# Performance work log

Hardware: AMD Instinct MI355X
Metric: run time of the kernel (lower is better)

The kernel has to match this reference:

```python
import jax, jax.numpy as jnp
import numpy as np

B, T, F, H, P, HEADS = 1024, 128, 9, 256, 2048, 4
DH = H // HEADS

def _lstm_layer(x, Wih, Whh, bih, bhh):
    # x: [B,T,in]; gate order i,f,g,o (torch convention)
    xp = jnp.einsum('bti,gi->btg', x, Wih) + bih + bhh  # [B,T,4H]
    h0 = jnp.zeros((x.shape[0], Whh.shape[1]), x.dtype)
    def step(carry, xt):
        h, c = carry
        g = xt + h @ Whh.T
        i, f, gg, o = jnp.split(g, 4, axis=-1)
        c = jax.nn.sigmoid(f) * c + jax.nn.sigmoid(i) * jnp.tanh(gg)
        h = jax.nn.sigmoid(o) * jnp.tanh(c)
        return (h, c), h
    _, hs = jax.lax.scan(step, (h0, h0), jnp.swapaxes(xp, 0, 1))
    return jnp.swapaxes(hs, 0, 1)  # [B,T,H]

def _layernorm(x, g, b, eps=1e-5):
    mu = x.mean(-1, keepdims=True)
    var = ((x - mu) ** 2).mean(-1, keepdims=True)
    return (x - mu) * jax.lax.rsqrt(var + eps) * g + b

def setup_inputs():
    key = jax.random.key(0)
    ks = jax.random.split(key, 30)
    w = lambda k, s: jax.random.normal(k, s, jnp.float32) * 0.05
    return {
        'x': jax.random.normal(ks[0], (B, T, F), jnp.float32),
        'sku_indices': jnp.arange(B, dtype=jnp.int32),
        'adj': jax.random.uniform(ks[1], (P, P), jnp.float32),
        'vsn_emb_w': w(ks[2], (F, H)), 'vsn_emb_b': w(ks[3], (F, H)),
        'vsn_sel_w': w(ks[4], (F, F)), 'vsn_sel_b': w(ks[5], (F,)),
        'lstm_Wih0': w(ks[6], (4 * H, H)), 'lstm_Whh0': w(ks[7], (4 * H, H)),
        'lstm_bih0': w(ks[8], (4 * H,)), 'lstm_bhh0': w(ks[9], (4 * H,)),
        'lstm_Wih1': w(ks[10], (4 * H, H)), 'lstm_Whh1': w(ks[11], (4 * H, H)),
        'lstm_bih1': w(ks[12], (4 * H,)), 'lstm_bhh1': w(ks[13], (4 * H,)),
        'attn_in_w': w(ks[14], (3 * H, H)), 'attn_in_b': w(ks[15], (3 * H,)),
        'attn_out_w': w(ks[16], (H, H)), 'attn_out_b': w(ks[17], (H,)),
        'gnn_w': w(ks[18], (H, H)), 'gnn_b': w(ks[19], (H,)),
        'ln_g': jnp.ones((H,), jnp.float32), 'ln_b': jnp.zeros((H,), jnp.float32),
        'gate_w': w(ks[20], (H, 2 * H)), 'gate_b': w(ks[21], (H,)),
        'out_w': w(ks[22], (1, H)), 'out_b': w(ks[23], (1,)),
    }

def reference(x, sku_indices, adj, vsn_emb_w, vsn_emb_b, vsn_sel_w, vsn_sel_b,
              lstm_Wih0, lstm_Whh0, lstm_bih0, lstm_bhh0,
              lstm_Wih1, lstm_Whh1, lstm_bih1, lstm_bhh1,
              attn_in_w, attn_in_b, attn_out_w, attn_out_b,
              gnn_w, gnn_b, ln_g, ln_b, gate_w, gate_b, out_w, out_b):
    # --- TFT hidden: variable selection -> 2-layer LSTM -> MHA, take last step ---
    emb = x[..., None] * vsn_emb_w + vsn_emb_b           # [B,T,F,H]
    wts = jax.nn.softmax(x @ vsn_sel_w.T + vsn_sel_b, -1)  # [B,T,F]
    h = jnp.einsum('btf,btfh->bth', wts, emb)            # [B,T,H]
    h = _lstm_layer(h, lstm_Wih0, lstm_Whh0, lstm_bih0, lstm_bhh0)
    h = _lstm_layer(h, lstm_Wih1, lstm_Whh1, lstm_bih1, lstm_bhh1)
    qkv = h @ attn_in_w.T + attn_in_b                    # [B,T,3H]
    q, k, v = [a.reshape(B, T, HEADS, DH) for a in jnp.split(qkv, 3, axis=-1)]
    scores = jnp.einsum('bqhd,bkhd->bhqk', q, k) / np.sqrt(DH).astype(np.float32)
    attn = jax.nn.softmax(scores, -1)
    o = jnp.einsum('bhqk,bkhd->bqhd', attn, v).reshape(B, T, H)
    o = o @ attn_out_w.T + attn_out_b
    hidden = o[:, -1, :]                                  # [B,H]
    # --- GNN enrichment (all sku_indices valid here) ---
    product_embeds = jnp.zeros((P, H), hidden.dtype).at[sku_indices].set(hidden)
    degree = jnp.clip(adj.sum(1, keepdims=True), 1e-6)
    aggregated = (adj / degree) @ product_embeds          # [P,H]
    transformed = jax.nn.gelu(aggregated @ gnn_w.T + gnn_b, approximate=False)
    transformed = _layernorm(transformed, ln_g, ln_b)
    enriched = transformed[sku_indices]                   # [B,H]
    gate = jax.nn.sigmoid(jnp.concatenate([hidden, enriched], -1) @ gate_w.T + gate_b)
    combined = gate * enriched + (1.0 - gate) * hidden
    out = combined @ out_w.T + out_b                      # [B,1]
    return out.squeeze(-1)
```

## Files before the change

kernel.cpp:

```cpp
#include <hip/hip_runtime.h>
#include <hip/hip_fp16.h>

typedef _Float16 f16;
typedef _Float16 f16x8 __attribute__((ext_vector_type(8)));
typedef _Float16 f16x4 __attribute__((ext_vector_type(4)));
typedef float f32x4 __attribute__((ext_vector_type(4)));

#define B_ 1024
#define T_ 128
#define F_ 9
#define H_ 256
#define P_ 2048

typedef unsigned long long ull;
#define AL(p) __hip_atomic_load((p), __ATOMIC_RELAXED, __HIP_MEMORY_SCOPE_AGENT)
#define AS(p, v) __hip_atomic_store((p), (v), __ATOMIC_RELAXED, __HIP_MEMORY_SCOPE_AGENT)

__device__ __forceinline__ float sigf(float x) { return 1.f / (1.f + __expf(-x)); }
__device__ __forceinline__ float tanh_(float x) {
  float a = fminf(fabsf(x), 12.f);
  float e = __expf(2.f * a);
  float r = 1.f - 2.f / (e + 1.f);
  return copysignf(r, x);
}

__device__ __forceinline__ f16x8 aload16(const f16* p) {
  union { ull u[2]; f16x8 v; } r;
  r.u[0] = AL((const ull*)p);
  r.u[1] = AL((const ull*)p + 1);
  return r.v;
}

__device__ __forceinline__ float blk_sum(float v) {
  __shared__ float sh[8];
  int lane = threadIdx.x & 63, w = threadIdx.x >> 6;
  int nw = blockDim.x >> 6;
#pragma unroll
  for (int o = 32; o > 0; o >>= 1) v += __shfl_xor(v, o, 64);
  __syncthreads();
  if (lane == 0) sh[w] = v;
  __syncthreads();
  float t = 0.f;
  for (int i = 0; i < nw; i++) t += sh[i];
  return t;
}

__global__ __launch_bounds__(256) void gemm_f16(
    const f16* __restrict__ A, int lda,
    const f16* __restrict__ Bt, int ldb,
    const float* __restrict__ bias,
    f16* __restrict__ o16, int ldo16,
    float* __restrict__ o32, int ldo32,
    f16* __restrict__ o16t, int ldt,
    int M, int N, int K)
{
  __shared__ __align__(16) f16 As[128][40];
  __shared__ __align__(16) f16 Bs[128][40];
  const int tid = threadIdx.x;
  const int lane = tid & 63, wave = tid >> 6;
  const int wr = (wave >> 1) * 64, wc = (wave & 1) * 64;
  const int q = lane >> 4, l15 = lane & 15;
  const int bm = blockIdx.x * 128, bn = blockIdx.y * 128;

  f32x4 acc[4][4];
#pragma unroll
  for (int i = 0; i < 4; i++)
#pragma unroll
    for (int j = 0; j < 4; j++) acc[i][j] = (f32x4){0.f, 0.f, 0.f, 0.f};

  for (int k0 = 0; k0 < K; k0 += 32) {
#pragma unroll
    for (int c = 0; c < 2; ++c) {
      int ch = tid + c * 256;
      int row = ch >> 2, kh = (ch & 3) * 8;
      *(f16x8*)&As[row][kh] = *(const f16x8*)&A[(size_t)(bm + row) * lda + k0 + kh];
      *(f16x8*)&Bs[row][kh] = *(const f16x8*)&Bt[(size_t)(bn + row) * ldb + k0 + kh];
    }
    __syncthreads();
    f16x8 af[4], bf[4];
#pragma unroll
    for (int tm = 0; tm < 4; tm++) af[tm] = *(const f16x8*)&As[wr + tm * 16 + l15][q * 8];
#pragma unroll
    for (int tn = 0; tn < 4; tn++) bf[tn] = *(const f16x8*)&Bs[wc + tn * 16 + l15][q * 8];
#pragma unroll
    for (int tm = 0; tm < 4; tm++)
#pragma unroll
      for (int tn = 0; tn < 4; tn++)
        acc[tm][tn] = __builtin_amdgcn_mfma_f32_16x16x32_f16(af[tm], bf[tn], acc[tm][tn], 0, 0, 0);
    __syncthreads();
  }
#pragma unroll
  for (int tm = 0; tm < 4; tm++) {
#pragma unroll
    for (int tn = 0; tn < 4; tn++) {
      int colg = bn + wc + tn * 16 + l15;
      float bv = bias ? bias[colg] : 0.f;
#pragma unroll
      for (int r = 0; r < 4; r++) {
        int rowg = bm + wr + tm * 16 + q * 4 + r;
        float v = acc[tm][tn][r] + bv;
        if (o32) o32[(size_t)rowg * ldo32 + colg] = v;
        if (o16) o16[(size_t)rowg * ldo16 + colg] = (f16)v;
        if (o16t) o16t[(size_t)colg * ldt + rowg] = (f16)v;
      }
    }
  }
}

__global__ __launch_bounds__(256, 1) void lstm_pipe(
    f16* __restrict__ hio,
    const f16* __restrict__ wpk0, const f16* __restrict__ wpk1,
    const float* __restrict__ b0, const float* __restrict__ b1,
    int* __restrict__ cnt0, int* __restrict__ cnt1)
{
  __shared__ __align__(16) f16 apf[2][16][64][8];
  __shared__ __align__(16) f16 htile[32][64];
  const int tid = threadIdx.x;
  const int lane = tid & 63, w = tid >> 6;
  const int q = lane >> 4, l15 = lane & 15;
  const int layer = blockIdx.x >> 7;
  const int lbid = blockIdx.x & 127;
  const int grp = lbid & 31, s = lbid >> 5;
  const int m0 = grp * 32;
  const f16* wpk = layer ? wpk1 : wpk0;
  const float* bias = layer ? b1 : b0;
  int* myflags = (layer ? cnt1 : cnt0) + grp * 64;
  int* xflags  = cnt0 + grp * 64;

  const int own0 = ((w >> 1) == s);
  const int own1 = (((w + 4) >> 1) == s);
  const int offh = (w & 1) * 32;

  f16x8 bf[4][16];
  {
    const f16* wbase = wpk + (((size_t)(s * 4 + w) * 4) * 16) * 512 + lane * 8;
#pragma unroll
    for (int g = 0; g < 4; g++)
#pragma unroll
      for (int k = 0; k < 16; k++)
        bf[g][k] = *(const f16x8*)(wbase + (size_t)(g * 16 + k) * 512);
  }
  float bv[4];
#pragma unroll
  for (int g = 0; g < 4; g++) bv[g] = bias[g * 256 + s * 64 + w * 16 + l15];

  const int srow = lane & 15, scb = lane >> 4;
  size_t rb[2];
  rb[0] = ((size_t)(m0 + srow) * T_) * 256 + scb * 8;
  rb[1] = ((size_t)(m0 + 16 + srow) * T_) * 256 + scb * 8;

  const f16x8 zv = {(f16)0, (f16)0, (f16)0, (f16)0, (f16)0, (f16)0, (f16)0, (f16)0};

  if (layer) {
    if (tid == 0) {
      int it = 0;
      for (;;) {
        ull a = AL((ull*)xflags);
        ull b2 = AL((ull*)xflags + 1);
        if ((int)a >= 2 && (int)(a >> 32) >= 2 &&
            (int)b2 >= 2 && (int)(b2 >> 32) >= 2) break;
        __builtin_amdgcn_s_sleep(1);
        if (++it > (1 << 22)) break;
      }
    }
    __syncthreads();
  }
  f16x8 xr[2][2];
#pragma unroll
  for (int mt = 0; mt < 2; mt++) {
    if (layer) {
      xr[mt][0] = aload16(&hio[rb[mt] + (size_t)w * 32]);
      xr[mt][1] = aload16(&hio[rb[mt] + (size_t)(w + 4) * 32]);
    } else {
      xr[mt][0] = *(const f16x8*)&hio[rb[mt] + (size_t)w * 32];
      xr[mt][1] = *(const f16x8*)&hio[rb[mt] + (size_t)(w + 4) * 32];
    }
  }
  float cst[2][4] = {{0.f, 0.f, 0.f, 0.f}, {0.f, 0.f, 0.f, 0.f}};

  __syncthreads();
  if (tid == 0) AS(&myflags[s], 1);

  for (int t = 0; t < T_; ++t) {
    if (tid == 0) {
      const int needO = t + 1;
      int needX = 0;
      if (layer) { needX = t + 3; if (needX > T_ + 1) needX = T_ + 1; }
      int it = 0;
      for (;;) {
        ull a = AL((ull*)myflags);
        ull b2 = AL((ull*)myflags + 1);
        bool ok = (int)a >= needO && (int)(a >> 32) >= needO &&
                  (int)b2 >= needO && (int)(b2 >> 32) >= needO;
        if (ok && layer) {
          ull c = AL((ull*)xflags);
          ull d = AL((ull*)xflags + 1);
          ok = (int)c >= needX && (int)(c >> 32) >= needX &&
               (int)d >= needX && (int)(d >> 32) >= needX;
        }
        if (ok) break;
        __builtin_amdgcn_s_sleep(1);
        if (++it > (1 << 22)) break;
      }
    }
    __syncthreads();

#pragma unroll
    for (int mt = 0; mt < 2; mt++) {
      *(f16x8*)&apf[mt][w][lane][0]     = xr[mt][0];
      *(f16x8*)&apf[mt][w + 4][lane][0] = xr[mt][1];
      f16x8 h0 = zv, h1 = zv;
      if (t > 0) {
        if (own0) h0 = *(const f16x8*)&htile[mt * 16 + srow][offh + scb * 8];
        else      h0 = aload16(&hio[rb[mt] + (size_t)(t - 1) * 256 + (size_t)w * 32]);
        if (own1) h1 = *(const f16x8*)&htile[mt * 16 + srow][offh + scb * 8];
        else      h1 = aload16(&hio[rb[mt] + (size_t)(t - 1) * 256 + (size_t)(w + 4) * 32]);
      }
      *(f16x8*)&apf[mt][8 + w][lane][0]  = h0;
      *(f16x8*)&apf[mt][12 + w][lane][0] = h1;
    }
    __syncthreads();

    f32x4 acc[2][4];
#pragma unroll
    for (int mt = 0; mt < 2; mt++)
#pragma unroll
      for (int g = 0; g < 4; g++) acc[mt][g] = (f32x4){0.f, 0.f, 0.f, 0.f};
#pragma unroll
    for (int k = 0; k < 16; k++) {
      f16x8 a0 = *(const f16x8*)&apf[0][k][lane][0];
      f16x8 a1 = *(const f16x8*)&apf[1][k][lane][0];
#pragma unroll
      for (int g = 0; g < 4; g++) {
        acc[0][g] = __builtin_amdgcn_mfma_f32_16x16x32_f16(a0, bf[g][k], acc[0][g], 0, 0, 0);
        acc[1][g] = __builtin_amdgcn_mfma_f32_16x16x32_f16(a1, bf[g][k], acc[1][g], 0, 0, 0);
      }
    }
    if (t + 1 < T_) {
#pragma unroll
      for (int mt = 0; mt < 2; mt++) {
        if (layer) {
          xr[mt][0] = aload16(&hio[rb[mt] + (size_t)(t + 1) * 256 + (size_t)w * 32]);
          xr[mt][1] = aload16(&hio[rb[mt] + (size_t)(t + 1) * 256 + (size_t)(w + 4) * 32]);
        } else {
          xr[mt][0] = *(const f16x8*)&hio[rb[mt] + (size_t)(t + 1) * 256 + (size_t)w * 32];
          xr[mt][1] = *(const f16x8*)&hio[rb[mt] + (size_t)(t + 1) * 256 + (size_t)(w + 4) * 32];
        }
      }
    }
    f16 hn[2][4];
#pragma unroll
    for (int mt = 0; mt < 2; mt++)
#pragma unroll
      for (int r = 0; r < 4; r++) {
        float ip = acc[mt][0][r] + bv[0];
        float fp = acc[mt][1][r] + bv[1];
        float gp = acc[mt][2][r] + bv[2];
        float op = acc[mt][3][r] + bv[3];
        float cn = sigf(fp) * cst[mt][r] + sigf(ip) * tanh_(gp);
        cst[mt][r] = cn;
        hn[mt][r] = (f16)(sigf(op) * tanh_(cn));
      }
#pragma unroll
    for (int mt = 0; mt < 2; mt++)
#pragma unroll
      for (int r = 0; r < 4; r++)
        htile[mt * 16 + q * 4 + r][w * 16 + l15] = hn[mt][r];
    __syncthreads();
    {
      int row = tid >> 3, c8 = (tid & 7) * 8;
      union { ull u[2]; f16x8 v; } uh;
      uh.v = *(const f16x8*)&htile[row][c8];
      ull* dst =
          (ull*)&hio[((size_t)(m0 + row) * T_ + t) * 256 + s * 64 + c8];
      AS(dst, uh.u[0]);
      AS(dst + 1, uh.u[1]);
    }
    __syncthreads();
    if (tid == 0) AS(&myflags[s], t + 2);
  }
}

__global__ __launch_bounds__(256) void vsn_w_kernel(
    const float* __restrict__ x, const float* __restrict__ selw,
    const float* __restrict__ selb, float* __restrict__ wb)
{
  int pos = blockIdx.x * 256 + threadIdx.x;
  const float* xr = x + (size_t)pos * F_;
  float xv[F_];
#pragma unroll
  for (int f = 0; f < F_; f++) xv[f] = xr[f];
  float wv[F_]; float mx = -1e30f;
#pragma unroll
  for (int f = 0; f < F_; f++) {
    float s = selb[f];
#pragma unroll
    for (int f2 = 0; f2 < F_; f2++) s += xv[f2] * selw[f * F_ + f2];
    wv[f] = s; mx = fmaxf(mx, s);
  }
  float se = 0.f;
#pragma unroll
  for (int f = 0; f < F_; f++) { wv[f] = __expf(wv[f] - mx); se += wv[f]; }
  float inv = 1.f / se;
  float* o = wb + (size_t)pos * 18;
#pragma unroll
  for (int f = 0; f < F_; f++) {
    float wt = wv[f] * inv;
    o[f] = wt; o[9 + f] = wt * xv[f];
  }
}

__global__ __launch_bounds__(256) void vsn_h_kernel(
    const float* __restrict__ wb, const float* __restrict__ embw,
    const float* __restrict__ embb, f16* __restrict__ hout)
{
  int j = threadIdx.x;
  float ew[F_], eb[F_];
#pragma unroll
  for (int f = 0; f < F_; f++) { ew[f] = embw[f * H_ + j]; eb[f] = embb[f * H_ + j]; }
  for (int i = 0; i < 128; i++) {
    size_t pos = blockIdx.x + (size_t)i * 1024;
    const float* w = wb + pos * 18;
    float h = 0.f;
#pragma unroll
    for (int f = 0; f < F_; f++) h += w[9 + f] * ew[f] + w[f] * eb[f];
    hout[pos * H_ + j] = (f16)h;
  }
}

__global__ __launch_bounds__(256) void attn_fused_kernel(
    const f16* __restrict__ hseq, const float* __restrict__ qbuf,
    const float* __restrict__ attn_in_w, const float* __restrict__ attn_in_b,
    f16* __restrict__ aob)
{
  __shared__ __align__(16) f16 hs[T_][264];
  __shared__ float qs[256];
  __shared__ float qks[4][256];
  __shared__ float ps[4][T_];
  __shared__ float hb[4][256];
  int b = blockIdx.x, tid = threadIdx.x;
  for (int i = tid; i < T_ * 32; i += 256) {
    int row = i >> 5, cc = (i & 31) * 8;
    *(f16x8*)&hs[row][cc] = *(const f16x8*)&hseq[((size_t)b * T_ + row) * 256 + cc];
  }
  qs[tid] = qbuf[(size_t)b * 256 + tid];
  __syncthreads();
  {
    int j = tid;
#pragma unroll
    for (int h = 0; h < 4; h++) {
      float acc = 0.f;
      for (int d = 0; d < 64; d++)
        acc += qs[h * 64 + d] * attn_in_w[(size_t)(256 + h * 64 + d) * 256 + j];
      qks[h][j] = acc * 0.125f;
    }
  }
  __syncthreads();
  if (tid < T_) {
    float s[4] = {0.f, 0.f, 0.f, 0.f};
    for (int cc = 0; cc < 32; cc++) {
      f16x8 v = *(const f16x8*)&hs[tid][cc * 8];
#pragma unroll
      for (int h = 0; h < 4; h++) {
        float a = 0.f;
#pragma unroll
        for (int j = 0; j < 8; j++) a += qks[h][cc * 8 + j] * (float)v[j];
        s[h] += a;
      }
    }
#pragma unroll
    for (int h = 0; h < 4; h++) ps[h][tid] = s[h];
  }
  __syncthreads();
  {
    int w = tid >> 6, l = tid & 63;
    float a = ps[w][l], bb = ps[w][l + 64];
    float m = fmaxf(a, bb);
#pragma unroll
    for (int o = 32; o > 0; o >>= 1) m = fmaxf(m, __shfl_xor(m, o, 64));
    float e0 = __expf(a - m), e1 = __expf(bb - m);
    float se = e0 + e1;
#pragma unroll
    for (int o = 32; o > 0; o >>= 1) se += __shfl_xor(se, o, 64);
    float inv = 1.f / se;
    ps[w][l] = e0 * inv; ps[w][l + 64] = e1 * inv;
  }
  __syncthreads();
  {
    int j = tid;
    float acc[4] = {0.f, 0.f, 0.f, 0.f};
    for (int t = 0; t < T_; t++) {
      float hv = (float)hs[t][j];
#pragma unroll
      for (int h = 0; h < 4; h++) acc[h] += ps[h][t] * hv;
    }
#pragma unroll
    for (int h = 0; h < 4; h++) hb[h][j] = acc[h];
  }
  __syncthreads();
  {
    int d = tid, h = d >> 6;
    const float4* wr = (const float4*)(attn_in_w + (size_t)(512 + d) * 256);
    float acc = 0.f;
    for (int cc = 0; cc < 64; cc++) {
      float4 w4 = wr[cc];
      acc += w4.x * hb[h][cc * 4] + w4.y * hb[h][cc * 4 + 1]
           + w4.z * hb[h][cc * 4 + 2] + w4.w * hb[h][cc * 4 + 3];
    }
    aob[(size_t)b * 256 + d] = (f16)(acc + attn_in_b[512 + d]);
  }
}

__global__ __launch_bounds__(256) void deg_adjn_kernel(
    const float* __restrict__ adj, const int* __restrict__ sku,
    f16* __restrict__ adjn)
{
  int bp = blockIdx.x;
  int p = sku[bp];
  int tid = threadIdx.x;
  float s = 0.f;
  for (int j = tid; j < P_; j += 256) s += adj[(size_t)p * P_ + j];
  float tot = blk_sum(s);
  float inv = 1.f / fmaxf(tot, 1e-6f);
  for (int b = tid; b < B_; b += 256)
    adjn[(size_t)bp * B_ + b] = (f16)(adj[(size_t)p * P_ + sku[b]] * inv);
}

__global__ __launch_bounds__(256) void gelu_ln_kernel(
    const float* __restrict__ pre, const float* __restrict__ lg,
    const float* __restrict__ lb, float* __restrict__ enr,
    f16* __restrict__ hidcat)
{
  int row = blockIdx.x, j = threadIdx.x;
  float xv = pre[row * 256 + j];
  float ge = 0.5f * xv * (1.f + erff(xv * 0.70710678118654752f));
  float mu = blk_sum(ge) * (1.f / 256.f);
  float d = ge - mu;
  float var = blk_sum(d * d) * (1.f / 256.f);
  float y = d * rsqrtf(var + 1e-5f) * lg[j] + lb[j];
  enr[row * 256 + j] = y;
  hidcat[row * 512 + 256 + j] = (f16)y;
}

__global__ __launch_bounds__(256) void final_kernel(
    const float* __restrict__ gpre, const float* __restrict__ enr,
    const float* __restrict__ hid, const float* __restrict__ outw,
    const float* __restrict__ outb, float* __restrict__ out)
{
  int b = blockIdx.x, j = threadIdx.x;
  float gt = sigf(gpre[b * 256 + j]);
  float comb = gt * enr[b * 256 + j] + (1.f - gt) * hid[b * 256 + j];
  float v = comb * outw[j];
  float s = blk_sum(v);
  if (j == 0) out[b] = s + outb[0];
}

__global__ void prep_kernel(
    const float* Wih0, const float* Whh0, const float* Wih1, const float* Whh1,
    const float* bih0, const float* bhh0, const float* bih1, const float* bhh1,
    const float* attn_in_w, const float* attn_out_w, const float* gnn_w,
    const float* gate_w,
    f16* wpk0, f16* wpk1, f16* attninf, f16* attnoutf, f16* gnnwf, f16* gatewf,
    float* bias0, float* bias1, int* flagz)
{
  int idx = blockIdx.x * 256 + threadIdx.x;
  if (idx < 524288) {
    int j = idx & 7, lane = (idx >> 3) & 63, k = (idx >> 9) & 15;
    int g = (idx >> 13) & 3, w = (idx >> 15) & 3, s = (idx >> 17) & 3;
    int row = g * 256 + s * 64 + w * 16 + (lane & 15);
    int col = k * 32 + (lane >> 4) * 8 + j;
    float v0 = col < 256 ? Wih0[(size_t)row * 256 + col] : Whh0[(size_t)row * 256 + col - 256];
    float v1 = col < 256 ? Wih1[(size_t)row * 256 + col] : Whh1[(size_t)row * 256 + col - 256];
    wpk0[idx] = (f16)v0;
    wpk1[idx] = (f16)v1;
    return;
  }
  int i = idx - 524288;
  if (i < 65536) { attninf[i] = (f16)attn_in_w[i]; return; }
  i -= 65536;
  if (i < 65536) { attnoutf[i] = (f16)attn_out_w[i]; return; }
  i -= 65536;
  if (i < 65536) { gnnwf[i] = (f16)gnn_w[i]; return; }
  i -= 65536;
  if (i < 131072) { gatewf[i] = (f16)gate_w[i]; return; }
  i -= 131072;
  if (i < 1024) { bias0[i] = bih0[i] + bhh0[i]; return; }
  i -= 1024;
  if (i < 1024) { bias1[i] = bih1[i] + bhh1[i]; return; }
  i -= 1024;
  if (i < 4096) { flagz[i] = 0; return; }
}

extern "C" void kernel_launch(void* const* d_in, const int* in_sizes, int n_in,
                              void* d_out, int out_size, void* d_ws, size_t ws_size,
                              hipStream_t stream)
{
  const float* x         = (const float*)d_in[0];
  const int*   sku       = (const int*)  d_in[1];
  const float* adj       = (const float*)d_in[2];
  const float* vsn_emb_w = (const float*)d_in[3];
  const float* vsn_emb_b = (const float*)d_in[4];
  const float* vsn_sel_w = (const float*)d_in[5];
  const float* vsn_sel_b = (const float*)d_in[6];
  const float* Wih0 = (const float*)d_in[7];
  const float* Whh0 = (const float*)d_in[8];
  const float* bih0 = (const float*)d_in[9];
  const float* bhh0 = (const float*)d_in[10];
  const float* Wih1 = (const float*)d_in[11];
  const float* Whh1 = (const float*)d_in[12];
  const float* bih1 = (const float*)d_in[13];
  const float* bhh1 = (const float*)d_in[14];
  const float* attn_in_w  = (const float*)d_in[15];
  const float* attn_in_b  = (const float*)d_in[16];
  const float* attn_out_w = (const float*)d_in[17];
  const float* attn_out_b = (const float*)d_in[18];
  const float* gnn_w  = (const float*)d_in[19];
  const float* gnn_b  = (const float*)d_in[20];
  const float* ln_g   = (const float*)d_in[21];
  const float* ln_b   = (const float*)d_in[22];
  const float* gate_w = (const float*)d_in[23];
  const float* gate_b = (const float*)d_in[24];
  const float* out_w  = (const float*)d_in[25];
  const float* out_b  = (const float*)d_in[26];
  (void)in_sizes; (void)n_in; (void)out_size; (void)ws_size;

  char* wsb = (char*)d_ws;
  size_t off = 0;
  auto alloc = [&](size_t bytes) -> void* {
    void* p = wsb + off;
    off += (bytes + 255) & ~(size_t)255;
    return p;
  };
  f16* hA      = (f16*)alloc((size_t)B_ * T_ * H_ * 2);
  f16* wpk0    = (f16*)alloc((size_t)1024 * 512 * 2);
  f16* wpk1    = (f16*)alloc((size_t)1024 * 512 * 2);
  f16* attninf = (f16*)alloc((size_t)256 * 256 * 2);
  f16* attnoutf= (f16*)alloc((size_t)256 * 256 * 2);
  f16* gnnwf   = (f16*)alloc((size_t)256 * 256 * 2);
  f16* gatewf  = (f16*)alloc((size_t)256 * 512 * 2);
  float* bias0 = (float*)alloc(1024 * 4);
  float* bias1 = (float*)alloc(1024 * 4);
  int* cnt0    = (int*)alloc(32 * 64 * 4);
  int* cnt1    = (int*)alloc(32 * 64 * 4);
  size_t off_tail = off;
  float* qbuf  = (float*)alloc((size_t)B_ * 256 * 4);
  f16* aob     = (f16*)alloc((size_t)B_ * 256 * 2);
  float* hidden32 = (float*)alloc((size_t)B_ * 256 * 4);
  f16* hidcat  = (f16*)alloc((size_t)B_ * 512 * 2);
  f16* hT      = (f16*)alloc((size_t)256 * B_ * 2);
  f16* adjn    = (f16*)alloc((size_t)B_ * B_ * 2);
  f16* aggf    = (f16*)alloc((size_t)B_ * 256 * 2);
  float* gnnpre= (float*)alloc((size_t)B_ * 256 * 4);
  float* enr32 = (float*)alloc((size_t)B_ * 256 * 4);
  float* gatepre=(float*)alloc((size_t)B_ * 256 * 4);
  float* wb    = (float*)(wsb + off_tail);

  prep_kernel<<<3353, 256, 0, stream>>>(
      Wih0, Whh0, Wih1, Whh1, bih0, bhh0, bih1, bhh1,
      attn_in_w, attn_out_w, gnn_w, gate_w,
      wpk0, wpk1, attninf, attnoutf, gnnwf, gatewf, bias0, bias1, cnt0);

  vsn_w_kernel<<<512, 256, 0, stream>>>(x, vsn_sel_w, vsn_sel_b, wb);
  vsn_h_kernel<<<1024, 256, 0, stream>>>(wb, vsn_emb_w, vsn_emb_b, hA);
  lstm_pipe<<<256, 256, 0, stream>>>(hA, wpk0, wpk1, bias0, bias1, cnt0, cnt1);

  dim3 gS(B_ / 128, 256 / 128);
  gemm_f16<<<gS, 256, 0, stream>>>(hA + (size_t)(T_ - 1) * 256, T_ * 256, attninf, 256,
                                   attn_in_b, nullptr, 0, qbuf, 256, nullptr, 0,
                                   B_, 256, 256);
  attn_fused_kernel<<<B_, 256, 0, stream>>>(hA, qbuf, attn_in_w, attn_in_b, aob);
  gemm_f16<<<gS, 256, 0, stream>>>(aob, 256, attnoutf, 256, attn_out_b,
                                   hidcat, 512, hidden32, 256, hT, B_,
                                   B_, 256, 256);
  deg_adjn_kernel<<<B_, 256, 0, stream>>>(adj, sku, adjn);
  gemm_f16<<<gS, 256, 0, stream>>>(adjn, 1024, hT, 1024, nullptr,
                                   aggf, 256, nullptr, 0, nullptr, 0,
                                   B_, 256, 1024);
  gemm_f16<<<gS, 256, 0, stream>>>(aggf, 256, gnnwf, 256, gnn_b,
                                   nullptr, 0, gnnpre, 256, nullptr, 0,
                                   B_, 256, 256);
  gelu_ln_kernel<<<B_, 256, 0, stream>>>(gnnpre, ln_g, ln_b, enr32, hidcat);
  gemm_f16<<<gS, 256, 0, stream>>>(hidcat, 512, gatewf, 512, gate_b,
                                   nullptr, 0, gatepre, 256, nullptr, 0,
                                   B_, 256, 512);
  final_kernel<<<B_, 256, 0, stream>>>(gatepre, enr32, hidden32, out_w, out_b, (float*)d_out);
}
```

Baseline: 998.7 us.

## Shrink GEMM tiles to 64x64, fuse VSN kernels, fold adjacency normalization into prep

The GEMM kernel moves from 128x128 tiles to 64x64 tiles, so each of the small M=1024,N=256 GEMMs launches 64 blocks instead of 16 and fills more CUs. The two VSN kernels become one, with the selection weights kept in shared memory instead of a global scratch buffer. The degree/adjacency normalization now runs as extra blocks of the prep kernel, which removes one launch and takes it off the post-LSTM critical path. The cost is less operand reuse per block in the GEMMs and a larger prep grid.

```diff
diff --git a/kernel.cpp b/kernel.cpp
--- a/kernel.cpp
+++ b/kernel.cpp
@@ -45,7 +45,7 @@
   return t;
 }
 
-__global__ __launch_bounds__(256) void gemm_f16(
+__global__ __launch_bounds__(256) void gemm64(
     const f16* __restrict__ A, int lda,
     const f16* __restrict__ Bt, int ldb,
     const float* __restrict__ bias,
@@ -54,55 +54,41 @@
     f16* __restrict__ o16t, int ldt,
     int M, int N, int K)
 {
-  __shared__ __align__(16) f16 As[128][40];
-  __shared__ __align__(16) f16 Bs[128][40];
+  __shared__ __align__(16) f16 As[64][40];
+  __shared__ __align__(16) f16 Bs[64][40];
   const int tid = threadIdx.x;
   const int lane = tid & 63, wave = tid >> 6;
-  const int wr = (wave >> 1) * 64, wc = (wave & 1) * 64;
   const int q = lane >> 4, l15 = lane & 15;
-  const int bm = blockIdx.x * 128, bn = blockIdx.y * 128;
-
-  f32x4 acc[4][4];
-#pragma unroll
-  for (int i = 0; i < 4; i++)
-#pragma unroll
-    for (int j = 0; j < 4; j++) acc[i][j] = (f32x4){0.f, 0.f, 0.f, 0.f};
+  const int bm = blockIdx.x * 64, bn = blockIdx.y * 64;
+
+  f32x4 acc[4];
+#pragma unroll
+  for (int tn = 0; tn < 4; tn++) acc[tn] = (f32x4){0.f, 0.f, 0.f, 0.f};
 
   for (int k0 = 0; k0 < K; k0 += 32) {
-#pragma unroll
-    for (int c = 0; c < 2; ++c) {
-      int ch = tid + c * 256;
-      int row = ch >> 2, kh = (ch & 3) * 8;
-      *(f16x8*)&As[row][kh] = *(const f16x8*)&A[(size_t)(bm + row) * lda + k0 + kh];
-      *(f16x8*)&Bs[row][kh] = *(const f16x8*)&Bt[(size_t)(bn + row) * ldb + k0 + kh];
-    }
-    __syncthreads();
-    f16x8 af[4], bf[4];
-#pragma unroll
-    for (int tm = 0; tm < 4; tm++) af[tm] = *(const f16x8*)&As[wr + tm * 16 + l15][q * 8];
-#pragma unroll
-    for (int tn = 0; tn < 4; tn++) bf[tn] = *(const f16x8*)&Bs[wc + tn * 16 + l15][q * 8];
-#pragma unroll
-    for (int tm = 0; tm < 4; tm++)
-#pragma unroll
-      for (int tn = 0; tn < 4; tn++)
-        acc[tm][tn] = __builtin_amdgcn_mfma_f32_16x16x32_f16(af[tm], bf[tn], acc[tm][tn], 0, 0, 0);
-    __syncthreads();
-  }
-#pragma unroll
-  for (int tm = 0; tm < 4; tm++) {
+    int row = tid >> 2, kh = (tid & 3) * 8;
+    *(f16x8*)&As[row][kh] = *(const f16x8*)&A[(size_t)(bm + row) * lda + k0 + kh];
+    *(f16x8*)&Bs[row][kh] = *(const f16x8*)&Bt[(size_t)(bn + row) * ldb + k0 + kh];
+    __syncthreads();
+    f16x8 af = *(const f16x8*)&As[wave * 16 + l15][q * 8];
 #pragma unroll
     for (int tn = 0; tn < 4; tn++) {
-      int colg = bn + wc + tn * 16 + l15;
-      float bv = bias ? bias[colg] : 0.f;
-#pragma unroll
-      for (int r = 0; r < 4; r++) {
-        int rowg = bm + wr + tm * 16 + q * 4 + r;
-        float v = acc[tm][tn][r] + bv;
-        if (o32) o32[(size_t)rowg * ldo32 + colg] = v;
-        if (o16) o16[(size_t)rowg * ldo16 + colg] = (f16)v;
-        if (o16t) o16t[(size_t)colg * ldt + rowg] = (f16)v;
-      }
+      f16x8 bf = *(const f16x8*)&Bs[tn * 16 + l15][q * 8];
+      acc[tn] = __builtin_amdgcn_mfma_f32_16x16x32_f16(af, bf, acc[tn], 0, 0, 0);
+    }
+    __syncthreads();
+  }
+#pragma unroll
+  for (int tn = 0; tn < 4; tn++) {
+    int colg = bn + tn * 16 + l15;
+    float bv = bias ? bias[colg] : 0.f;
+#pragma unroll
+    for (int r = 0; r < 4; r++) {
+      int rowg = bm + wave * 16 + q * 4 + r;
+      float v = acc[tn][r] + bv;
+      if (o32) o32[(size_t)rowg * ldo32 + colg] = v;
+      if (o16) o16[(size_t)rowg * ldo16 + colg] = (f16)v;
+      if (o16t) o16t[(size_t)colg * ldt + rowg] = (f16)v;
     }
   }
 }
@@ -281,50 +267,47 @@
   }
 }
 
-__global__ __launch_bounds__(256) void vsn_w_kernel(
+__global__ __launch_bounds__(256) void vsn_fused_kernel(
     const float* __restrict__ x, const float* __restrict__ selw,
-    const float* __restrict__ selb, float* __restrict__ wb)
-{
-  int pos = blockIdx.x * 256 + threadIdx.x;
-  const float* xr = x + (size_t)pos * F_;
-  float xv[F_];
-#pragma unroll
-  for (int f = 0; f < F_; f++) xv[f] = xr[f];
-  float wv[F_]; float mx = -1e30f;
-#pragma unroll
-  for (int f = 0; f < F_; f++) {
-    float s = selb[f];
-#pragma unroll
-    for (int f2 = 0; f2 < F_; f2++) s += xv[f2] * selw[f * F_ + f2];
-    wv[f] = s; mx = fmaxf(mx, s);
-  }
-  float se = 0.f;
-#pragma unroll
-  for (int f = 0; f < F_; f++) { wv[f] = __expf(wv[f] - mx); se += wv[f]; }
-  float inv = 1.f / se;
-  float* o = wb + (size_t)pos * 18;
-#pragma unroll
-  for (int f = 0; f < F_; f++) {
-    float wt = wv[f] * inv;
-    o[f] = wt; o[9 + f] = wt * xv[f];
-  }
-}
-
-__global__ __launch_bounds__(256) void vsn_h_kernel(
-    const float* __restrict__ wb, const float* __restrict__ embw,
+    const float* __restrict__ selb, const float* __restrict__ embw,
     const float* __restrict__ embb, f16* __restrict__ hout)
 {
-  int j = threadIdx.x;
+  __shared__ float wbs[128][18];
+  int b = blockIdx.x, tid = threadIdx.x;
+  if (tid < 128) {
+    size_t pos = (size_t)b * 128 + tid;
+    const float* xr = x + pos * F_;
+    float xv[F_];
+#pragma unroll
+    for (int f = 0; f < F_; f++) xv[f] = xr[f];
+    float wv[F_]; float mx = -1e30f;
+#pragma unroll
+    for (int f = 0; f < F_; f++) {
+      float s = selb[f];
+#pragma unroll
+      for (int f2 = 0; f2 < F_; f2++) s += xv[f2] * selw[f * F_ + f2];
+      wv[f] = s; mx = fmaxf(mx, s);
+    }
+    float se = 0.f;
+#pragma unroll
+    for (int f = 0; f < F_; f++) { wv[f] = __expf(wv[f] - mx); se += wv[f]; }
+    float inv = 1.f / se;
+#pragma unroll
+    for (int f = 0; f < F_; f++) {
+      float wt = wv[f] * inv;
+      wbs[tid][f] = wt; wbs[tid][9 + f] = wt * xv[f];
+    }
+  }
+  __syncthreads();
+  int j = tid;
   float ew[F_], eb[F_];
 #pragma unroll
   for (int f = 0; f < F_; f++) { ew[f] = embw[f * H_ + j]; eb[f] = embb[f * H_ + j]; }
   for (int i = 0; i < 128; i++) {
-    size_t pos = blockIdx.x + (size_t)i * 1024;
-    const float* w = wb + pos * 18;
     float h = 0.f;
 #pragma unroll
-    for (int f = 0; f < F_; f++) h += w[9 + f] * ew[f] + w[f] * eb[f];
-    hout[pos * H_ + j] = (f16)h;
+    for (int f = 0; f < F_; f++) h += wbs[i][9 + f] * ew[f] + wbs[i][f] * eb[f];
+    hout[((size_t)b * 128 + i) * H_ + j] = (f16)h;
   }
 }
 
@@ -411,21 +394,6 @@
   }
 }
 
-__global__ __launch_bounds__(256) void deg_adjn_kernel(
-    const float* __restrict__ adj, const int* __restrict__ sku,
-    f16* __restrict__ adjn)
-{
-  int bp = blockIdx.x;
-  int p = sku[bp];
-  int tid = threadIdx.x;
-  float s = 0.f;
-  for (int j = tid; j < P_; j += 256) s += adj[(size_t)p * P_ + j];
-  float tot = blk_sum(s);
-  float inv = 1.f / fmaxf(tot, 1e-6f);
-  for (int b = tid; b < B_; b += 256)
-    adjn[(size_t)bp * B_ + b] = (f16)(adj[(size_t)p * P_ + sku[b]] * inv);
-}
-
 __global__ __launch_bounds__(256) void gelu_ln_kernel(
     const float* __restrict__ pre, const float* __restrict__ lg,
     const float* __restrict__ lb, float* __restrict__ enr,
@@ -459,10 +427,22 @@
     const float* Wih0, const float* Whh0, const float* Wih1, const float* Whh1,
     const float* bih0, const float* bhh0, const float* bih1, const float* bhh1,
     const float* attn_in_w, const float* attn_out_w, const float* gnn_w,
-    const float* gate_w,
+    const float* gate_w, const float* adj, const int* sku,
     f16* wpk0, f16* wpk1, f16* attninf, f16* attnoutf, f16* gnnwf, f16* gatewf,
-    float* bias0, float* bias1, int* flagz)
-{
+    float* bias0, float* bias1, int* flagz, f16* adjn)
+{
+  if (blockIdx.x >= 3353) {
+    int bp = blockIdx.x - 3353;
+    int p = sku[bp];
+    int tid = threadIdx.x;
+    float s = 0.f;
+    for (int j = tid; j < P_; j += 256) s += adj[(size_t)p * P_ + j];
+    float tot = blk_sum(s);
+    float inv = 1.f / fmaxf(tot, 1e-6f);
+    for (int b = tid; b < B_; b += 256)
+      adjn[(size_t)bp * B_ + b] = (f16)(adj[(size_t)p * P_ + sku[b]] * inv);
+    return;
+  }
   int idx = blockIdx.x * 256 + threadIdx.x;
   if (idx < 524288) {
     int j = idx & 7, lane = (idx >> 3) & 63, k = (idx >> 9) & 15;
@@ -542,46 +522,43 @@
   float* bias1 = (float*)alloc(1024 * 4);
   int* cnt0    = (int*)alloc(32 * 64 * 4);
   int* cnt1    = (int*)alloc(32 * 64 * 4);
-  size_t off_tail = off;
+  f16* adjn    = (f16*)alloc((size_t)B_ * B_ * 2);
   float* qbuf  = (float*)alloc((size_t)B_ * 256 * 4);
   f16* aob     = (f16*)alloc((size_t)B_ * 256 * 2);
   float* hidden32 = (float*)alloc((size_t)B_ * 256 * 4);
   f16* hidcat  = (f16*)alloc((size_t)B_ * 512 * 2);
   f16* hT      = (f16*)alloc((size_t)256 * B_ * 2);
-  f16* adjn    = (f16*)alloc((size_t)B_ * B_ * 2);
   f16* aggf    = (f16*)alloc((size_t)B_ * 256 * 2);
   float* gnnpre= (float*)alloc((size_t)B_ * 256 * 4);
   float* enr32 = (float*)alloc((size_t)B_ * 256 * 4);
   float* gatepre=(float*)alloc((size_t)B_ * 256 * 4);
-  float* wb    = (float*)(wsb + off_tail);
-
-  prep_kernel<<<3353, 256, 0, stream>>>(
+
+  prep_kernel<<<4377, 256, 0, stream>>>(
       Wih0, Whh0, Wih1, Whh1, bih0, bhh0, bih1, bhh1,
-      attn_in_w, attn_out_w, gnn_w, gate_w,
-      wpk0, wpk1, attninf, attnoutf, gnnwf, gatewf, bias0, bias1, cnt0);
-
-  vsn_w_kernel<<<512, 256, 0, stream>>>(x, vsn_sel_w, vsn_sel_b, wb);
-  vsn_h_kernel<<<1024, 256, 0, stream>>>(wb, vsn_emb_w, vsn_emb_b, hA);
+      attn_in_w, attn_out_w, gnn_w, gate_w, adj, sku,
+      wpk0, wpk1, attninf, attnoutf, gnnwf, gatewf, bias0, bias1, cnt0, adjn);
+
+  vsn_fused_kernel<<<B_, 256, 0, stream>>>(x, vsn_sel_w, vsn_sel_b,
+                                           vsn_emb_w, vsn_emb_b, hA);
   lstm_pipe<<<256, 256, 0, stream>>>(hA, wpk0, wpk1, bias0, bias1, cnt0, cnt1);
 
-  dim3 gS(B_ / 128, 256 / 128);
-  gemm_f16<<<gS, 256, 0, stream>>>(hA + (size_t)(T_ - 1) * 256, T_ * 256, attninf, 256,
-                                   attn_in_b, nullptr, 0, qbuf, 256, nullptr, 0,
-                                   B_, 256, 256);
+  dim3 g64(B_ / 64, 256 / 64);
+  gemm64<<<g64, 256, 0, stream>>>(hA + (size_t)(T_ - 1) * 256, T_ * 256, attninf, 256,
+                                  attn_in_b, nullptr, 0, qbuf, 256, nullptr, 0,
+                                  B_, 256, 256);
   attn_fused_kernel<<<B_, 256, 0, stream>>>(hA, qbuf, attn_in_w, attn_in_b, aob);
-  gemm_f16<<<gS, 256, 0, stream>>>(aob, 256, attnoutf, 256, attn_out_b,
-                                   hidcat, 512, hidden32, 256, hT, B_,
-                                   B_, 256, 256);
-  deg_adjn_kernel<<<B_, 256, 0, stream>>>(adj, sku, adjn);
-  gemm_f16<<<gS, 256, 0, stream>>>(adjn, 1024, hT, 1024, nullptr,
-                                   aggf, 256, nullptr, 0, nullptr, 0,
-                                   B_, 256, 1024);
-  gemm_f16<<<gS, 256, 0, stream>>>(aggf, 256, gnnwf, 256, gnn_b,
-                                   nullptr, 0, gnnpre, 256, nullptr, 0,
-                                   B_, 256, 256);
+  gemm64<<<g64, 256, 0, stream>>>(aob, 256, attnoutf, 256, attn_out_b,
+                                  hidcat, 512, hidden32, 256, hT, B_,
+                                  B_, 256, 256);
+  gemm64<<<g64, 256, 0, stream>>>(adjn, 1024, hT, 1024, nullptr,
+                                  aggf, 256, nullptr, 0, nullptr, 0,
+                                  B_, 256, 1024);
+  gemm64<<<g64, 256, 0, stream>>>(aggf, 256, gnnwf, 256, gnn_b,
+                                  nullptr, 0, gnnpre, 256, nullptr, 0,
+                                  B_, 256, 256);
   gelu_ln_kernel<<<B_, 256, 0, stream>>>(gnnpre, ln_g, ln_b, enr32, hidcat);
-  gemm_f16<<<gS, 256, 0, stream>>>(hidcat, 512, gatewf, 512, gate_b,
-                                   nullptr, 0, gatepre, 256, nullptr, 0,
-                                   B_, 256, 512);
+  gemm64<<<g64, 256, 0, stream>>>(hidcat, 512, gatewf, 512, gate_b,
+                                  nullptr, 0, gatepre, 256, nullptr, 0,
+                                  B_, 256, 512);
   final_kernel<<<B_, 256, 0, stream>>>(gatepre, enr32, hidden32, out_w, out_b, (float*)d_out);
 }
```

Result: faster. 951.0 us (-4.8%).
